# Kernel optimization log

Hardware: AMD Instinct MI355X
Metric: run time of the kernel (lower is better)

The kernel has to match this reference:

```python
import jax, jax.numpy as jnp
import numpy as np

WS = 7       # window_size
NH = 4       # num_head = dim_in // dim_head
HD = 64      # dim_head
ALPHA = 0.1
BETA = 0.2
THETA = 0.5
EPS = 1e-5   # LayerNorm eps


def dwconv(x, w):
    # x: [b, C, h, w], w: [C, 1, k, k] depthwise, padding 'same', no bias
    return jax.lax.conv_general_dilated(
        x, w, window_strides=(1, 1), padding='SAME',
        feature_group_count=x.shape[1],
        dimension_numbers=('NCHW', 'OIHW', 'NCHW'))


def setup_inputs() -> dict:
    key = jax.random.key(0)
    ks = jax.random.split(key, 8)
    B, H, W, C = 32, 56, 56, 256
    s = 0.02
    return {
        'x': jax.random.normal(ks[0], (B, H, W, C), jnp.float32),
        'qkv_w': jax.random.normal(ks[1], (3 * C, C), jnp.float32) * s,
        'qkv_b': jnp.zeros((3 * C,), jnp.float32),
        'conv3_w': jax.random.normal(ks[2], (C, 1, 3, 3), jnp.float32) * s,
        'conv5_w': jax.random.normal(ks[3], (C, 1, 5, 5), jnp.float32) * s,
        'conv7_w': jax.random.normal(ks[4], (C, 1, 7, 7), jnp.float32) * s,
        'ffn_in_w': jax.random.normal(ks[5], (C, C), jnp.float32) * s,
        'ffn_out_w': jax.random.normal(ks[6], (C, C), jnp.float32) * s,
        'ln_g': jnp.ones((C,), jnp.float32),
        'ln_b': jnp.zeros((C,), jnp.float32),
    }


def reference(x, qkv_w, qkv_b, conv3_w, conv5_w, conv7_w, ffn_in_w, ffn_out_w, ln_g, ln_b):
    B, H, W, C = x.shape
    n1, n2 = H // WS, W // WS  # H,W divisible by WS -> no padding path
    # rearrange 'b (h1 n1) (w1 n2) c -> (b n1 n2) h1 w1 c' (window dim is MAJOR axis)
    xw = x.reshape(B, WS, n1, WS, n2, C).transpose(0, 2, 4, 1, 3, 5)
    xw = xw.reshape(B * n1 * n2, WS, WS, C)
    b, hw = B * n1 * n2, WS * WS

    shortcut = xw.reshape(b, hw, NH, HD).transpose(0, 2, 1, 3)  # [b, nh, hw, hd]
    qkv = xw.reshape(b, hw, C) @ qkv_w.T + qkv_b                # [b, hw, 3C]
    qkv = qkv.reshape(b, hw, 3, NH, HD).transpose(2, 0, 3, 1, 4)
    q, k, v = qkv[0], qkv[1], qkv[2]
    v = ALPHA * v + shortcut                                     # scaled residual into V
    shortcut2 = v.transpose(0, 2, 1, 3).reshape(b, WS, WS, C)    # [b, h, w, C]

    # SDPA with default scale hd^-0.5
    attn = jax.nn.softmax(jnp.einsum('bnqd,bnkd->bnqk', q, k) * (HD ** -0.5), axis=-1)
    x_spa = jnp.einsum('bnqk,bnkd->bnqd', attn, v)
    x_spa = x_spa.transpose(0, 2, 1, 3).reshape(b, WS, WS, C)

    # conv branches on modified v: v.transpose(-1,-2).reshape(b, C, h, w)
    xc = v.transpose(0, 1, 3, 2).reshape(b, C, WS, WS)
    c3 = dwconv(xc, conv3_w).transpose(0, 2, 3, 1)
    c5 = dwconv(xc, conv5_w).transpose(0, 2, 3, 1)
    c7 = dwconv(xc, conv7_w).transpose(0, 2, 3, 1)
    x_spa = 0.25 * (x_spa + c3 + c5 + c7)  # equal 0.25 branch weights

    xw = BETA * x_spa + shortcut2
    # inverse rearrange '(b n1 n2) h1 w1 c -> b (h1 n1) (w1 n2) c'
    xo = xw.reshape(B, n1, n2, WS, WS, C).transpose(0, 3, 1, 4, 2, 5).reshape(B, H, W, C)

    # FFN (bias=False) with scaled residual, then LayerNorm
    y = jax.nn.silu(xo @ ffn_in_w.T) @ ffn_out_w.T
    xo = THETA * y + xo
    mu = jnp.mean(xo, axis=-1, keepdims=True)
    var = jnp.var(xo, axis=-1, keepdims=True)
    return (xo - mu) / jnp.sqrt(var + EPS) * ln_g + ln_b
```

## Files before the change

### kernel.cpp

```cpp
#include <hip/hip_runtime.h>

typedef unsigned short u16;
typedef unsigned short u16x8 __attribute__((ext_vector_type(8)));
typedef unsigned short u16x4 __attribute__((ext_vector_type(4)));
typedef unsigned int   u32x2 __attribute__((ext_vector_type(2)));
typedef short          s16x8 __attribute__((ext_vector_type(8)));
typedef float          f32x4 __attribute__((ext_vector_type(4)));

#define DEV static __device__ __forceinline__

DEV float bf2f(u16 u){ unsigned int v = ((unsigned int)u) << 16; return __builtin_bit_cast(float, v); }
DEV u16 f2bf(float f){
  unsigned int u = __builtin_bit_cast(unsigned int, f);
  u += 0x7fffu + ((u >> 16) & 1u);
  return (u16)(u >> 16);
}

DEV f32x4 mfma16(u16x8 a, u16x8 b, f32x4 c){
  return __builtin_amdgcn_mfma_f32_16x16x32_bf16(
      __builtin_bit_cast(s16x8, a), __builtin_bit_cast(s16x8, b), c, 0, 0, 0);
}

DEV void g2l16(const void* g, void* l){
  __builtin_amdgcn_global_load_lds((const __attribute__((address_space(1))) void*)g,
                                   (__attribute__((address_space(3))) void*)l, 16, 0, 0);
}

DEV size_t xrow_from(int b, int hw){
  int h1 = hw / 7, w1 = hw - h1 * 7;
  return ((size_t)(((b >> 6) * 56 + h1 * 8 + ((b >> 3) & 7)) * 56 + (w1 * 8 + (b & 7)))) << 8;
}
DEV size_t xrow_off(int t){ int b = t / 49; return xrow_from(b, t - b * 49); }

__global__ __launch_bounds__(256) void k_prep(const float* __restrict__ qkvw,
                                              const float* __restrict__ c3,
                                              const float* __restrict__ c5,
                                              const float* __restrict__ c7,
                                              const float* __restrict__ fin,
                                              const float* __restrict__ fout,
                                              u16* __restrict__ wq, u16* __restrict__ wfi,
                                              u16* __restrict__ wfo, float* __restrict__ weff){
  int id = blockIdx.x * 256 + threadIdx.x;
  if (id < 196608) { wq[id] = f2bf(qkvw[id]); return; }
  id -= 196608;
  if (id < 65536) { wfi[id] = f2bf(fin[id]); return; }
  id -= 65536;
  if (id < 65536) { wfo[id] = f2bf(fout[id]); return; }
  id -= 65536;
  if (id < 12544) {
    int c = id / 49, t = id - c * 49;
    int di = t / 7 - 3, dj = t % 7 - 3;
    float s = c7[c * 49 + t];
    if (di >= -2 && di <= 2 && dj >= -2 && dj <= 2) s += c5[c * 25 + (di + 2) * 5 + (dj + 2)];
    if (di >= -1 && di <= 1 && dj >= -1 && dj <= 1) s += c3[c * 9 + (di + 1) * 3 + (dj + 1)];
    weff[t * 256 + c] = 0.05f * s;
  }
}

__global__ __launch_bounds__(256) void k_xbf(const float* __restrict__ x, u16* __restrict__ xbf){
  int tid = threadIdx.x;
  int tok = blockIdx.x * 4 + (tid >> 6);
  int c4 = (tid & 63) * 4;
  float4 v = *(const float4*)(x + xrow_off(tok) + c4);
  u16x4 o; o[0] = f2bf(v.x); o[1] = f2bf(v.y); o[2] = f2bf(v.z); o[3] = f2bf(v.w);
  *(u16x4*)&xbf[(size_t)tok * 256 + c4] = o;
}

__global__ __launch_bounds__(256) void k_qkv(const u16* __restrict__ xbf,
                                             const u16* __restrict__ wq,
                                             const float* __restrict__ qkvb,
                                             u16* __restrict__ qb, u16* __restrict__ kb,
                                             u16* __restrict__ vmb){
  __shared__ __align__(16) u16 As[128 * 64];
  __shared__ __align__(16) u16 Bs[128 * 64];
  const int bid = blockIdx.x;
  const int lin = (bid & 7) * 588 + (bid >> 3);
  const int bm = lin / 6, bn = lin - bm * 6;
  const int tid = threadIdx.x, lane = tid & 63, wid = tid >> 6;
  const int wm = wid >> 1, wn = wid & 1;
  const int r = lane & 15, g = lane >> 4;
  const int lr = lane >> 3;
  const int swz = ((lane & 7) ^ lr) * 16;
  const f32x4 fz = {0.f, 0.f, 0.f, 0.f};
  f32x4 acc[4][4];
#pragma unroll
  for (int m = 0; m < 4; ++m)
#pragma unroll
    for (int n = 0; n < 4; ++n) acc[m][n] = fz;

  const char* gA0 = (const char*)xbf + (size_t)bm * 128 * 512;
  const char* gB0 = (const char*)wq  + (size_t)bn * 128 * 512;

  for (int kt = 0; kt < 4; ++kt) {
#pragma unroll
    for (int ri = 0; ri < 4; ++ri) {
      int chunk = ri * 4 + wid;
      int row = chunk * 8 + lr;
      g2l16(gA0 + (size_t)row * 512 + kt * 128 + swz, (char*)As + chunk * 1024);
      g2l16(gB0 + (size_t)row * 512 + kt * 128 + swz, (char*)Bs + chunk * 1024);
    }
    __syncthreads();
#pragma unroll
    for (int kk = 0; kk < 2; ++kk) {
      u16x8 af[4], bq[4];
#pragma unroll
      for (int m = 0; m < 4; ++m)
        af[m] = *(const u16x8*)&As[(wm * 64 + m * 16 + r) * 64 + (((kk * 4 + g) ^ (r & 7)) * 8)];
#pragma unroll
      for (int n = 0; n < 4; ++n)
        bq[n] = *(const u16x8*)&Bs[(wn * 64 + n * 16 + r) * 64 + (((kk * 4 + g) ^ (r & 7)) * 8)];
#pragma unroll
      for (int m = 0; m < 4; ++m)
#pragma unroll
        for (int n = 0; n < 4; ++n) acc[m][n] = mfma16(af[m], bq[n], acc[m][n]);
    }
    __syncthreads();
  }

  const int sec = bn >> 1;
  const int cb = (bn & 1) * 128 + wn * 64;
  u16* const outp = (sec == 0) ? qb : (sec == 1) ? kb : vmb;
  float bias[4];
#pragma unroll
  for (int n = 0; n < 4; ++n) bias[n] = qkvb[sec * 256 + cb + n * 16 + r];
#pragma unroll
  for (int m = 0; m < 4; ++m) {
#pragma unroll
    for (int i = 0; i < 4; ++i) {
      int t = bm * 128 + wm * 64 + m * 16 + g * 4 + i;
      u16* dst = outp + (size_t)t * 256 + cb;
      if (sec == 0) {
#pragma unroll
        for (int n = 0; n < 4; ++n) dst[n * 16 + r] = f2bf((acc[m][n][i] + bias[n]) * 0.125f);
      } else if (sec == 1) {
#pragma unroll
        for (int n = 0; n < 4; ++n) dst[n * 16 + r] = f2bf(acc[m][n][i] + bias[n]);
      } else {
        const u16* xsrc = xbf + (size_t)t * 256 + cb;
#pragma unroll
        for (int n = 0; n < 4; ++n)
          dst[n * 16 + r] = f2bf(0.1f * (acc[m][n][i] + bias[n]) + bf2f(xsrc[n * 16 + r]));
      }
    }
  }
}

template<int HW0, int NPIX>
DEV void conv_do(const float (&in_f)[49], const float (&wreg)[49], const u16* xs,
                 int c, size_t obase, u16* __restrict__ xo){
#pragma unroll
  for (int p = 0; p < NPIX; ++p) {
    const int hw = HW0 + p;
    const int i0 = hw / 7, j0 = hw % 7;
    float a = 0.f;
#pragma unroll
    for (int di = -3; di <= 3; ++di) {
      const int ii = i0 + di;
      if (ii < 0 || ii > 6) continue;
#pragma unroll
      for (int dj = -3; dj <= 3; ++dj) {
        const int jj = j0 + dj;
        if (jj < 0 || jj > 6) continue;
        a += in_f[ii * 7 + jj] * wreg[(di + 3) * 7 + (dj + 3)];
      }
    }
    float xsv = bf2f(xs[hw * 72 + c]);
    float outv = in_f[hw] + 0.05f * xsv + a;
    xo[obase + (size_t)hw * 128] = f2bf(outv);
  }
}

__global__ __launch_bounds__(256) void k_attn(const u16* __restrict__ qb,
                                              const u16* __restrict__ kb,
                                              const u16* __restrict__ vmb,
                                              const float* __restrict__ weff,
                                              u16* __restrict__ xo){
  __shared__ __align__(16) u16 smem[18432];
  const int bx = blockIdx.x;
  const int b = bx >> 1, hp = bx & 1;
  const int tid = threadIdx.x, lane = tid & 63, wid = tid >> 6;
  const int hl = wid >> 1, hf = wid & 1;
  const int hg = hp * 2 + hl;
  const int vto = hl * 9216, po = hl * 9216 + 4608;
  const int r = lane & 15, g = lane >> 4;
  const size_t tok0 = (size_t)b * 49;
  const int hc = hg * 64;

  if (hf == 0) {
    int c = lane;
    u16 pix[49];
#pragma unroll
    for (int hw = 0; hw < 49; ++hw) pix[hw] = vmb[(tok0 + hw) * 256 + hc + c];
#pragma unroll
    for (int t2 = 0; t2 < 12; ++t2) {
      u32x2 w;
      w[0] = (unsigned)pix[4 * t2] | ((unsigned)pix[4 * t2 + 1] << 16);
      w[1] = (unsigned)pix[4 * t2 + 2] | ((unsigned)pix[4 * t2 + 3] << 16);
      *(u32x2*)&smem[vto + c * 72 + 4 * t2] = w;
    }
    u32x2 wl; wl[0] = (unsigned)pix[48]; wl[1] = 0u;
    *(u32x2*)&smem[vto + c * 72 + 48] = wl;
    u32x2 z; z[0] = 0u; z[1] = 0u;
    *(u32x2*)&smem[vto + c * 72 + 52] = z;
    *(u32x2*)&smem[vto + c * 72 + 56] = z;
    *(u32x2*)&smem[vto + c * 72 + 60] = z;
  }

  const int mt0 = hf * 2;
  const f32x4 fz = {0.f, 0.f, 0.f, 0.f};
  f32x4 s[2][4];
#pragma unroll
  for (int m = 0; m < 2; ++m)
#pragma unroll
    for (int n = 0; n < 4; ++n) s[m][n] = fz;
  u16x8 aq[2][2], bk[4][2];
#pragma unroll
  for (int m = 0; m < 2; ++m) {
    int qrow = (mt0 + m) * 16 + r; if (qrow > 48) qrow = 48;
    const u16* src = qb + (tok0 + qrow) * 256 + hc;
    aq[m][0] = *(const u16x8*)(src + g * 8);
    aq[m][1] = *(const u16x8*)(src + 32 + g * 8);
  }
#pragma unroll
  for (int n = 0; n < 4; ++n) {
    int krow = n * 16 + r; if (krow > 48) krow = 0;
    const u16* src = kb + (tok0 + krow) * 256 + hc;
    bk[n][0] = *(const u16x8*)(src + g * 8);
    bk[n][1] = *(const u16x8*)(src + 32 + g * 8);
  }
#pragma unroll
  for (int kk = 0; kk < 2; ++kk)
#pragma unroll
    for (int m = 0; m < 2; ++m)
#pragma unroll
      for (int n = 0; n < 4; ++n) s[m][n] = mfma16(aq[m][kk], bk[n][kk], s[m][n]);

#pragma unroll
  for (int m = 0; m < 2; ++m) {
#pragma unroll
    for (int i = 0; i < 4; ++i) {
      float x0 = s[m][0][i], x1 = s[m][1][i], x2 = s[m][2][i];
      float x3 = (r >= 1) ? -1e30f : s[m][3][i];
      float mx = fmaxf(fmaxf(x0, x1), fmaxf(x2, x3));
#pragma unroll
      for (int off = 1; off < 16; off <<= 1) mx = fmaxf(mx, __shfl_xor(mx, off, 64));
      float e0 = __expf(x0 - mx), e1 = __expf(x1 - mx), e2 = __expf(x2 - mx);
      float e3 = (r >= 1) ? 0.f : __expf(x3 - mx);
      float sum = e0 + e1 + e2 + e3;
#pragma unroll
      for (int off = 1; off < 16; off <<= 1) sum += __shfl_xor(sum, off, 64);
      float inv = 1.f / sum;
      int rowp = po + ((mt0 + m) * 16 + g * 4 + i) * 72;
      smem[rowp + r]       = f2bf(e0 * inv);
      smem[rowp + 16 + r]  = f2bf(e1 * inv);
      smem[rowp + 32 + r]  = f2bf(e2 * inv);
      smem[rowp + 48 + r]  = f2bf(e3 * inv);
    }
  }
  __syncthreads();

  f32x4 o[2][4];
#pragma unroll
  for (int m = 0; m < 2; ++m)
#pragma unroll
    for (int n = 0; n < 4; ++n) o[m][n] = fz;
#pragma unroll
  for (int kk = 0; kk < 2; ++kk) {
    u16x8 pa[2], vb[4];
#pragma unroll
    for (int m = 0; m < 2; ++m) pa[m] = *(const u16x8*)&smem[po + ((mt0 + m) * 16 + r) * 72 + kk * 32 + g * 8];
#pragma unroll
    for (int n = 0; n < 4; ++n) vb[n] = *(const u16x8*)&smem[vto + (n * 16 + r) * 72 + kk * 32 + g * 8];
#pragma unroll
    for (int m = 0; m < 2; ++m)
#pragma unroll
      for (int n = 0; n < 4; ++n) o[m][n] = mfma16(pa[m], vb[n], o[m][n]);
  }
#pragma unroll
  for (int m = 0; m < 2; ++m)
#pragma unroll
    for (int n = 0; n < 4; ++n)
#pragma unroll
      for (int i = 0; i < 4; ++i)
        smem[po + ((mt0 + m) * 16 + g * 4 + i) * 72 + n * 16 + r] = f2bf(o[m][n][i]);
  __syncthreads();

  {
    int c = lane;
    float in_f[49];
#pragma unroll
    for (int t2 = 0; t2 < 6; ++t2) {
      u16x8 raw = *(const u16x8*)&smem[vto + c * 72 + t2 * 8];
#pragma unroll
      for (int e = 0; e < 8; ++e) in_f[t2 * 8 + e] = bf2f(raw[e]);
    }
    in_f[48] = bf2f(smem[vto + c * 72 + 48]);
    float wreg[49];
#pragma unroll
    for (int t2 = 0; t2 < 49; ++t2) wreg[t2] = weff[t2 * 256 + hg * 64 + c];
    size_t obase = (size_t)b * 12544 + (size_t)hp * 6272 + (size_t)(hl * 64 + c);
    if (hf == 0) conv_do<0, 25>(in_f, wreg, &smem[po], c, obase, xo);
    else         conv_do<25, 24>(in_f, wreg, &smem[po], c, obase, xo);
  }
}

__global__ __launch_bounds__(256) void k_ffn1(const u16* __restrict__ xo,
                                              const u16* __restrict__ wfi,
                                              u16* __restrict__ h){
  __shared__ __align__(16) u16 As[128 * 64];
  __shared__ __align__(16) u16 Bs[128 * 64];
  const int bid = blockIdx.x;
  const int lin = (bid & 7) * 196 + (bid >> 3);
  const int bm = lin >> 1, bn = lin & 1;
  const int tid = threadIdx.x, lane = tid & 63, wid = tid >> 6;
  const int wm = wid >> 1, wn = wid & 1;
  const int r = lane & 15, g = lane >> 4;
  const int lr = lane >> 3;
  const int swz = ((lane & 7) ^ lr) * 16;
  const f32x4 fz = {0.f, 0.f, 0.f, 0.f};
  f32x4 acc[4][4];
#pragma unroll
  for (int m = 0; m < 4; ++m)
#pragma unroll
    for (int n = 0; n < 4; ++n) acc[m][n] = fz;

  for (int kt = 0; kt < 4; ++kt) {
#pragma unroll
    for (int ri = 0; ri < 4; ++ri) {
      int chunk = ri * 4 + wid;
      int row = chunk * 8 + lr;
      int t = bm * 128 + row;
      int win = t / 49, hw = t - win * 49;
      size_t off = (size_t)win * 12544 + (size_t)(kt >> 1) * 6272 + (size_t)hw * 128 + (kt & 1) * 64;
      g2l16((const char*)xo + off * 2 + swz, (char*)As + chunk * 1024);
      g2l16((const char*)wfi + (size_t)(bn * 128 + row) * 512 + kt * 128 + swz, (char*)Bs + chunk * 1024);
    }
    __syncthreads();
#pragma unroll
    for (int kk = 0; kk < 2; ++kk) {
      u16x8 af[4], bq[4];
#pragma unroll
      for (int m = 0; m < 4; ++m)
        af[m] = *(const u16x8*)&As[(wm * 64 + m * 16 + r) * 64 + (((kk * 4 + g) ^ (r & 7)) * 8)];
#pragma unroll
      for (int n = 0; n < 4; ++n)
        bq[n] = *(const u16x8*)&Bs[(wn * 64 + n * 16 + r) * 64 + (((kk * 4 + g) ^ (r & 7)) * 8)];
#pragma unroll
      for (int m = 0; m < 4; ++m)
#pragma unroll
        for (int n = 0; n < 4; ++n) acc[m][n] = mfma16(af[m], bq[n], acc[m][n]);
    }
    __syncthreads();
  }
#pragma unroll
  for (int m = 0; m < 4; ++m)
#pragma unroll
    for (int i = 0; i < 4; ++i) {
      int t = bm * 128 + wm * 64 + m * 16 + g * 4 + i;
      u16* dst = h + (size_t)t * 256 + bn * 128 + wn * 64;
#pragma unroll
      for (int n = 0; n < 4; ++n) {
        float v = acc[m][n][i];
        float sg = v / (1.f + __expf(-v));
        dst[n * 16 + r] = f2bf(sg);
      }
    }
}

__global__ __launch_bounds__(512) void k_ffn2(const u16* __restrict__ h,
                                              const u16* __restrict__ wfo,
                                              const u16* __restrict__ xo,
                                              const float* __restrict__ lng,
                                              const float* __restrict__ lnb,
                                              float* __restrict__ out){
  __shared__ __align__(16) u16 As[128 * 64];
  __shared__ __align__(16) u16 Bs[256 * 64];
  __shared__ float red1[4][128];
  __shared__ float red2[4][128];
  const int bm = blockIdx.x;
  const int tid = threadIdx.x, lane = tid & 63, wid = tid >> 6;
  const int wm = wid >> 2, wn = wid & 3;
  const int r = lane & 15, g = lane >> 4;
  const int lr = lane >> 3;
  const int swz = ((lane & 7) ^ lr) * 16;
  const f32x4 fz = {0.f, 0.f, 0.f, 0.f};
  f32x4 acc[4][4];
#pragma unroll
  for (int m = 0; m < 4; ++m)
#pragma unroll
    for (int n = 0; n < 4; ++n) acc[m][n] = fz;

  for (int kt = 0; kt < 4; ++kt) {
#pragma unroll
    for (int ri = 0; ri < 2; ++ri) {
      int chunk = ri * 8 + wid;
      int row = chunk * 8 + lr;
      g2l16((const char*)h + (size_t)(bm * 128 + row) * 512 + kt * 128 + swz, (char*)As + chunk * 1024);
    }
#pragma unroll
    for (int ri = 0; ri < 4; ++ri) {
      int chunk = ri * 8 + wid;
      int row = chunk * 8 + lr;
      g2l16((const char*)wfo + (size_t)row * 512 + kt * 128 + swz, (char*)Bs + chunk * 1024);
    }
    __syncthreads();
#pragma unroll
    for (int kk = 0; kk < 2; ++kk) {
      u16x8 af[4], bq[4];
#pragma unroll
      for (int m = 0; m < 4; ++m)
        af[m] = *(const u16x8*)&As[(wm * 64 + m * 16 + r) * 64 + (((kk * 4 + g) ^ (r & 7)) * 8)];
#pragma unroll
      for (int n = 0; n < 4; ++n)
        bq[n] = *(const u16x8*)&Bs[(wn * 64 + n * 16 + r) * 64 + (((kk * 4 + g) ^ (r & 7)) * 8)];
#pragma unroll
      for (int m = 0; m < 4; ++m)
#pragma unroll
        for (int n = 0; n < 4; ++n) acc[m][n] = mfma16(af[m], bq[n], acc[m][n]);
    }
    __syncthreads();
  }

  float lg[4], lb[4];
#pragma unroll
  for (int n = 0; n < 4; ++n) {
    int col = wn * 64 + n * 16 + r;
    lg[n] = lng[col]; lb[n] = lnb[col];
  }
#pragma unroll
  for (int m = 0; m < 4; ++m)
#pragma unroll
    for (int i = 0; i < 4; ++i) {
      int t = bm * 128 + wm * 64 + m * 16 + g * 4 + i;
      int b49 = t / 49, hw = t - b49 * 49;
      size_t xbase = (size_t)b49 * 12544 + (size_t)hw * 128;
#pragma unroll
      for (int n = 0; n < 4; ++n) {
        int col = wn * 64 + n * 16 + r;
        acc[m][n][i] = 0.5f * acc[m][n][i] + bf2f(xo[xbase + (col >> 7) * 6272 + (col & 127)]);
      }
    }
#pragma unroll
  for (int m = 0; m < 4; ++m)
#pragma unroll
    for (int i = 0; i < 4; ++i) {
      float s1 = 0.f, s2 = 0.f;
#pragma unroll
      for (int n = 0; n < 4; ++n) { float v = acc[m][n][i]; s1 += v; s2 += v * v; }
#pragma unroll
      for (int off = 1; off < 16; off <<= 1) { s1 += __shfl_xor(s1, off, 64); s2 += __shfl_xor(s2, off, 64); }
      if (r == 0) {
        int rl = wm * 64 + m * 16 + g * 4 + i;
        red1[wn][rl] = s1; red2[wn][rl] = s2;
      }
    }
  __syncthreads();
#pragma unroll
  for (int m = 0; m < 4; ++m)
#pragma unroll
    for (int i = 0; i < 4; ++i) {
      int rl = wm * 64 + m * 16 + g * 4 + i;
      float S1 = red1[0][rl] + red1[1][rl] + red1[2][rl] + red1[3][rl];
      float S2 = red2[0][rl] + red2[1][rl] + red2[2][rl] + red2[3][rl];
      float mu = S1 * (1.f / 256.f);
      float var = S2 * (1.f / 256.f) - mu * mu;
      float rstd = rsqrtf(var + 1e-5f);
      int t = bm * 128 + rl;
      int b49 = t / 49, hw = t - b49 * 49;
      size_t ob = xrow_from(b49, hw);
#pragma unroll
      for (int n = 0; n < 4; ++n) {
        int col = wn * 64 + n * 16 + r;
        out[ob + col] = (acc[m][n][i] - mu) * rstd * lg[n] + lb[n];
      }
    }
}

extern "C" void kernel_launch(void* const* d_in, const int* in_sizes, int n_in,
                              void* d_out, int out_size, void* d_ws, size_t ws_size,
                              hipStream_t stream) {
  (void)in_sizes; (void)n_in; (void)out_size; (void)ws_size;
  const float* x     = (const float*)d_in[0];
  const float* qkvw  = (const float*)d_in[1];
  const float* qkvb  = (const float*)d_in[2];
  const float* c3    = (const float*)d_in[3];
  const float* c5    = (const float*)d_in[4];
  const float* c7    = (const float*)d_in[5];
  const float* fin   = (const float*)d_in[6];
  const float* fout  = (const float*)d_in[7];
  const float* lng   = (const float*)d_in[8];
  const float* lnb   = (const float*)d_in[9];
  float* out = (float*)d_out;
  char* ws = (char*)d_ws;

  u16*   qbuf = (u16*)(ws);
  u16*   kbuf = (u16*)(ws + 51380224);
  u16*   vmb  = (u16*)(ws + 102760448);
  u16*   wq   = (u16*)(ws + 154140672);
  u16*   wfi  = (u16*)(ws + 154533888);
  u16*   wfo  = (u16*)(ws + 154664960);
  float* weff = (float*)(ws + 154796032);
  u16*   xbf  = (u16*)d_out;

  k_prep<<<dim3(1329), dim3(256), 0, stream>>>(qkvw, c3, c5, c7, fin, fout, wq, wfi, wfo, weff);
  k_xbf<<<dim3(25088), dim3(256), 0, stream>>>(x, xbf);
  k_qkv<<<dim3(4704), dim3(256), 0, stream>>>(xbf, wq, qkvb, qbuf, kbuf, vmb);
  k_attn<<<dim3(4096), dim3(256), 0, stream>>>(qbuf, kbuf, vmb, weff, kbuf );
  k_ffn1<<<dim3(1568), dim3(256), 0, stream>>>(kbuf , wfi, qbuf );
  k_ffn2<<<dim3(784), dim3(512), 0, stream>>>(qbuf , wfo, kbuf , lng, lnb, out);
}
```

Baseline: 268.6 us.

## Fuse fp32-to-bf16 window gather into QKV GEMM and transpose conv weights

The separate k_xbf pass, which gathered window tokens from x and converted them to bf16, is removed. The QKV GEMM now loads fp32 rows of x directly, converts them to bf16 and writes them into swizzled LDS, and reads the V residual straight from fp32 x. Separately, the combined conv weights are stored per channel with a stride of 52, so the attention kernel can load them with float4 vector reads instead of 49 strided scalar loads. This drops one kernel launch and a full bf16 round trip of the activations. In exchange the GEMM A-tile load becomes synchronous register-staged fp32 traffic (twice the bytes) instead of async global-to-LDS copies, and the gathered rows are strided.

```diff
diff --git a/kernel.cpp b/kernel.cpp
--- a/kernel.cpp
+++ b/kernel.cpp
@@ -39,7 +39,7 @@
                                               const float* __restrict__ fin,
                                               const float* __restrict__ fout,
                                               u16* __restrict__ wq, u16* __restrict__ wfi,
-                                              u16* __restrict__ wfo, float* __restrict__ weff){
+                                              u16* __restrict__ wfo, float* __restrict__ weffT){
   int id = blockIdx.x * 256 + threadIdx.x;
   if (id < 196608) { wq[id] = f2bf(qkvw[id]); return; }
   id -= 196608;
@@ -53,20 +53,11 @@
     float s = c7[c * 49 + t];
     if (di >= -2 && di <= 2 && dj >= -2 && dj <= 2) s += c5[c * 25 + (di + 2) * 5 + (dj + 2)];
     if (di >= -1 && di <= 1 && dj >= -1 && dj <= 1) s += c3[c * 9 + (di + 1) * 3 + (dj + 1)];
-    weff[t * 256 + c] = 0.05f * s;
-  }
-}
-
-__global__ __launch_bounds__(256) void k_xbf(const float* __restrict__ x, u16* __restrict__ xbf){
-  int tid = threadIdx.x;
-  int tok = blockIdx.x * 4 + (tid >> 6);
-  int c4 = (tid & 63) * 4;
-  float4 v = *(const float4*)(x + xrow_off(tok) + c4);
-  u16x4 o; o[0] = f2bf(v.x); o[1] = f2bf(v.y); o[2] = f2bf(v.z); o[3] = f2bf(v.w);
-  *(u16x4*)&xbf[(size_t)tok * 256 + c4] = o;
-}
-
-__global__ __launch_bounds__(256) void k_qkv(const u16* __restrict__ xbf,
+    weffT[c * 52 + t] = 0.05f * s;
+  }
+}
+
+__global__ __launch_bounds__(256) void k_qkv(const float* __restrict__ x,
                                              const u16* __restrict__ wq,
                                              const float* __restrict__ qkvb,
                                              u16* __restrict__ qb, u16* __restrict__ kb,
@@ -88,16 +79,30 @@
 #pragma unroll
     for (int n = 0; n < 4; ++n) acc[m][n] = fz;
 
-  const char* gA0 = (const char*)xbf + (size_t)bm * 128 * 512;
-  const char* gB0 = (const char*)wq  + (size_t)bn * 128 * 512;
+  const int r0 = tid >> 1;
+  const int ch0 = (tid & 1) * 32;
+  const float* xsrc = x + xrow_off(bm * 128 + r0);
+  const char* gB0 = (const char*)wq + (size_t)bn * 128 * 512;
 
   for (int kt = 0; kt < 4; ++kt) {
 #pragma unroll
     for (int ri = 0; ri < 4; ++ri) {
       int chunk = ri * 4 + wid;
       int row = chunk * 8 + lr;
-      g2l16(gA0 + (size_t)row * 512 + kt * 128 + swz, (char*)As + chunk * 1024);
       g2l16(gB0 + (size_t)row * 512 + kt * 128 + swz, (char*)Bs + chunk * 1024);
+    }
+    {
+      float4 f[8];
+#pragma unroll
+      for (int j = 0; j < 8; ++j) f[j] = *(const float4*)(xsrc + kt * 64 + ch0 + j * 4);
+#pragma unroll
+      for (int j = 0; j < 4; ++j) {
+        u16x8 o;
+        o[0] = f2bf(f[j*2].x); o[1] = f2bf(f[j*2].y); o[2] = f2bf(f[j*2].z); o[3] = f2bf(f[j*2].w);
+        o[4] = f2bf(f[j*2+1].x); o[5] = f2bf(f[j*2+1].y); o[6] = f2bf(f[j*2+1].z); o[7] = f2bf(f[j*2+1].w);
+        int blk = (ch0 >> 3) + j;
+        *(u16x8*)&As[r0 * 64 + ((blk ^ (r0 & 7)) * 8)] = o;
+      }
     }
     __syncthreads();
 #pragma unroll
@@ -136,10 +141,10 @@
 #pragma unroll
         for (int n = 0; n < 4; ++n) dst[n * 16 + r] = f2bf(acc[m][n][i] + bias[n]);
       } else {
-        const u16* xsrc = xbf + (size_t)t * 256 + cb;
+        const float* xs2 = x + xrow_off(t) + cb;
 #pragma unroll
         for (int n = 0; n < 4; ++n)
-          dst[n * 16 + r] = f2bf(0.1f * (acc[m][n][i] + bias[n]) + bf2f(xsrc[n * 16 + r]));
+          dst[n * 16 + r] = f2bf(0.1f * (acc[m][n][i] + bias[n]) + xs2[n * 16 + r]);
       }
     }
   }
@@ -173,7 +178,7 @@
 __global__ __launch_bounds__(256) void k_attn(const u16* __restrict__ qb,
                                               const u16* __restrict__ kb,
                                               const u16* __restrict__ vmb,
-                                              const float* __restrict__ weff,
+                                              const float* __restrict__ weffT,
                                               u16* __restrict__ xo){
   __shared__ __align__(16) u16 smem[18432];
   const int bx = blockIdx.x;
@@ -296,8 +301,13 @@
     }
     in_f[48] = bf2f(smem[vto + c * 72 + 48]);
     float wreg[49];
-#pragma unroll
-    for (int t2 = 0; t2 < 49; ++t2) wreg[t2] = weff[t2 * 256 + hg * 64 + c];
+    const float* wsrc = weffT + (size_t)(hg * 64 + c) * 52;
+#pragma unroll
+    for (int j = 0; j < 12; ++j) {
+      float4 v = *(const float4*)(wsrc + j * 4);
+      wreg[j * 4] = v.x; wreg[j * 4 + 1] = v.y; wreg[j * 4 + 2] = v.z; wreg[j * 4 + 3] = v.w;
+    }
+    wreg[48] = wsrc[48];
     size_t obase = (size_t)b * 12544 + (size_t)hp * 6272 + (size_t)(hl * 64 + c);
     if (hf == 0) conv_do<0, 25>(in_f, wreg, &smem[po], c, obase, xo);
     else         conv_do<25, 24>(in_f, wreg, &smem[po], c, obase, xo);
@@ -493,19 +503,17 @@
   float* out = (float*)d_out;
   char* ws = (char*)d_ws;
 
-  u16*   qbuf = (u16*)(ws);
-  u16*   kbuf = (u16*)(ws + 51380224);
-  u16*   vmb  = (u16*)(ws + 102760448);
-  u16*   wq   = (u16*)(ws + 154140672);
-  u16*   wfi  = (u16*)(ws + 154533888);
-  u16*   wfo  = (u16*)(ws + 154664960);
-  float* weff = (float*)(ws + 154796032);
-  u16*   xbf  = (u16*)d_out;
-
-  k_prep<<<dim3(1329), dim3(256), 0, stream>>>(qkvw, c3, c5, c7, fin, fout, wq, wfi, wfo, weff);
-  k_xbf<<<dim3(25088), dim3(256), 0, stream>>>(x, xbf);
-  k_qkv<<<dim3(4704), dim3(256), 0, stream>>>(xbf, wq, qkvb, qbuf, kbuf, vmb);
-  k_attn<<<dim3(4096), dim3(256), 0, stream>>>(qbuf, kbuf, vmb, weff, kbuf );
+  u16*   qbuf  = (u16*)(ws);
+  u16*   kbuf  = (u16*)(ws + 51380224);
+  u16*   vmb   = (u16*)(ws + 102760448);
+  u16*   wq    = (u16*)(ws + 154140672);
+  u16*   wfi   = (u16*)(ws + 154533888);
+  u16*   wfo   = (u16*)(ws + 154664960);
+  float* weffT = (float*)(ws + 154796032);
+
+  k_prep<<<dim3(1329), dim3(256), 0, stream>>>(qkvw, c3, c5, c7, fin, fout, wq, wfi, wfo, weffT);
+  k_qkv<<<dim3(4704), dim3(256), 0, stream>>>(x, wq, qkvb, qbuf, kbuf, vmb);
+  k_attn<<<dim3(4096), dim3(256), 0, stream>>>(qbuf, kbuf, vmb, weffT, kbuf );
   k_ffn1<<<dim3(1568), dim3(256), 0, stream>>>(kbuf , wfi, qbuf );
   k_ffn2<<<dim3(784), dim3(512), 0, stream>>>(qbuf , wfo, kbuf , lng, lnb, out);
 }
```

Result: slower. 340.5 us (+26.8%).

## Store attention output token-major and transpose conv weights for vector loads

Applied to the files above, without the earlier changes.

The attention kernel's output changes from a split half-channel layout (two 128-channel planes per window) to plain token-major rows of 256 channels. This lets both FFN kernels address rows linearly instead of doing per-row divide-by-49 index math. The fused conv weights are also stored transposed per channel, padded to 52, so each thread loads its 49 taps with float4 vector loads instead of 49 strided scalar loads. The risk is that the attention store now scatters 2-byte writes at a 256-element stride per pixel.

```diff
diff --git a/kernel.cpp b/kernel.cpp
--- a/kernel.cpp
+++ b/kernel.cpp
@@ -39,7 +39,7 @@
                                               const float* __restrict__ fin,
                                               const float* __restrict__ fout,
                                               u16* __restrict__ wq, u16* __restrict__ wfi,
-                                              u16* __restrict__ wfo, float* __restrict__ weff){
+                                              u16* __restrict__ wfo, float* __restrict__ weffT){
   int id = blockIdx.x * 256 + threadIdx.x;
   if (id < 196608) { wq[id] = f2bf(qkvw[id]); return; }
   id -= 196608;
@@ -53,7 +53,7 @@
     float s = c7[c * 49 + t];
     if (di >= -2 && di <= 2 && dj >= -2 && dj <= 2) s += c5[c * 25 + (di + 2) * 5 + (dj + 2)];
     if (di >= -1 && di <= 1 && dj >= -1 && dj <= 1) s += c3[c * 9 + (di + 1) * 3 + (dj + 1)];
-    weff[t * 256 + c] = 0.05f * s;
+    weffT[c * 52 + t] = 0.05f * s;
   }
 }
 
@@ -166,14 +166,14 @@
     }
     float xsv = bf2f(xs[hw * 72 + c]);
     float outv = in_f[hw] + 0.05f * xsv + a;
-    xo[obase + (size_t)hw * 128] = f2bf(outv);
+    xo[obase + (size_t)hw * 256] = f2bf(outv);
   }
 }
 
 __global__ __launch_bounds__(256) void k_attn(const u16* __restrict__ qb,
                                               const u16* __restrict__ kb,
                                               const u16* __restrict__ vmb,
-                                              const float* __restrict__ weff,
+                                              const float* __restrict__ weffT,
                                               u16* __restrict__ xo){
   __shared__ __align__(16) u16 smem[18432];
   const int bx = blockIdx.x;
@@ -296,9 +296,14 @@
     }
     in_f[48] = bf2f(smem[vto + c * 72 + 48]);
     float wreg[49];
-#pragma unroll
-    for (int t2 = 0; t2 < 49; ++t2) wreg[t2] = weff[t2 * 256 + hg * 64 + c];
-    size_t obase = (size_t)b * 12544 + (size_t)hp * 6272 + (size_t)(hl * 64 + c);
+    const float* wsrc = weffT + (size_t)(hc + c) * 52;
+#pragma unroll
+    for (int j = 0; j < 12; ++j) {
+      float4 v = *(const float4*)(wsrc + j * 4);
+      wreg[j * 4] = v.x; wreg[j * 4 + 1] = v.y; wreg[j * 4 + 2] = v.z; wreg[j * 4 + 3] = v.w;
+    }
+    wreg[48] = wsrc[48];
+    size_t obase = tok0 * 256 + hc + c;
     if (hf == 0) conv_do<0, 25>(in_f, wreg, &smem[po], c, obase, xo);
     else         conv_do<25, 24>(in_f, wreg, &smem[po], c, obase, xo);
   }
@@ -324,16 +329,16 @@
 #pragma unroll
     for (int n = 0; n < 4; ++n) acc[m][n] = fz;
 
+  const char* gA0 = (const char*)xo + (size_t)bm * 128 * 512;
+  const char* gB0 = (const char*)wfi + (size_t)bn * 128 * 512;
+
   for (int kt = 0; kt < 4; ++kt) {
 #pragma unroll
     for (int ri = 0; ri < 4; ++ri) {
       int chunk = ri * 4 + wid;
       int row = chunk * 8 + lr;
-      int t = bm * 128 + row;
-      int win = t / 49, hw = t - win * 49;
-      size_t off = (size_t)win * 12544 + (size_t)(kt >> 1) * 6272 + (size_t)hw * 128 + (kt & 1) * 64;
-      g2l16((const char*)xo + off * 2 + swz, (char*)As + chunk * 1024);
-      g2l16((const char*)wfi + (size_t)(bn * 128 + row) * 512 + kt * 128 + swz, (char*)Bs + chunk * 1024);
+      g2l16(gA0 + (size_t)row * 512 + kt * 128 + swz, (char*)As + chunk * 1024);
+      g2l16(gB0 + (size_t)row * 512 + kt * 128 + swz, (char*)Bs + chunk * 1024);
     }
     __syncthreads();
 #pragma unroll
@@ -432,12 +437,11 @@
 #pragma unroll
     for (int i = 0; i < 4; ++i) {
       int t = bm * 128 + wm * 64 + m * 16 + g * 4 + i;
-      int b49 = t / 49, hw = t - b49 * 49;
-      size_t xbase = (size_t)b49 * 12544 + (size_t)hw * 128;
+      const u16* xsrc = xo + (size_t)t * 256;
 #pragma unroll
       for (int n = 0; n < 4; ++n) {
         int col = wn * 64 + n * 16 + r;
-        acc[m][n][i] = 0.5f * acc[m][n][i] + bf2f(xo[xbase + (col >> 7) * 6272 + (col & 127)]);
+        acc[m][n][i] = 0.5f * acc[m][n][i] + bf2f(xsrc[col]);
       }
     }
 #pragma unroll
@@ -493,19 +497,19 @@
   float* out = (float*)d_out;
   char* ws = (char*)d_ws;
 
-  u16*   qbuf = (u16*)(ws);
-  u16*   kbuf = (u16*)(ws + 51380224);
-  u16*   vmb  = (u16*)(ws + 102760448);
-  u16*   wq   = (u16*)(ws + 154140672);
-  u16*   wfi  = (u16*)(ws + 154533888);
-  u16*   wfo  = (u16*)(ws + 154664960);
-  float* weff = (float*)(ws + 154796032);
-  u16*   xbf  = (u16*)d_out;
-
-  k_prep<<<dim3(1329), dim3(256), 0, stream>>>(qkvw, c3, c5, c7, fin, fout, wq, wfi, wfo, weff);
+  u16*   qbuf  = (u16*)(ws);
+  u16*   kbuf  = (u16*)(ws + 51380224);
+  u16*   vmb   = (u16*)(ws + 102760448);
+  u16*   wq    = (u16*)(ws + 154140672);
+  u16*   wfi   = (u16*)(ws + 154533888);
+  u16*   wfo   = (u16*)(ws + 154664960);
+  float* weffT = (float*)(ws + 154796032);
+  u16*   xbf   = (u16*)d_out;
+
+  k_prep<<<dim3(1329), dim3(256), 0, stream>>>(qkvw, c3, c5, c7, fin, fout, wq, wfi, wfo, weffT);
   k_xbf<<<dim3(25088), dim3(256), 0, stream>>>(x, xbf);
   k_qkv<<<dim3(4704), dim3(256), 0, stream>>>(xbf, wq, qkvb, qbuf, kbuf, vmb);
-  k_attn<<<dim3(4096), dim3(256), 0, stream>>>(qbuf, kbuf, vmb, weff, kbuf );
+  k_attn<<<dim3(4096), dim3(256), 0, stream>>>(qbuf, kbuf, vmb, weffT, kbuf );
   k_ffn1<<<dim3(1568), dim3(256), 0, stream>>>(kbuf , wfi, qbuf );
   k_ffn2<<<dim3(784), dim3(512), 0, stream>>>(qbuf , wfo, kbuf , lng, lnb, out);
 }
```

New measurement: 264.5 us. Within noise of the previous version (-1.5%).
